# Kernel tuning notes

Measured on AMD Instinct MI355X. Metric: run time of the kernel, lower is better.

The kernel has to match this reference:

```python
import jax, jax.numpy as jnp
import numpy as np
import math

B, T, S = 8, 8, 64
L = T * S            # 512 tokens per modality
D = 1024             # bi_hidden_size
H = 16               # bi_num_attention_heads
DH = D // H          # 64 head size (queries)
DKV = D // 2         # 512 kv projection size
SCALE = 1.0 / math.sqrt(DH)


def setup_inputs() -> dict:
    key = jax.random.key(0)
    ks = jax.random.split(key, 24)
    inp = {
        "input_tensor1": jax.random.normal(ks[0], (B, T, S, D), jnp.float32),
        "attention_mask1": jnp.zeros((B, 1, 1, L), jnp.float32),
        "input_tensor2": jax.random.normal(ks[1], (B, T, S, D), jnp.float32),
        "attention_mask2": jnp.zeros((B, 1, 1, L), jnp.float32),
        "input_tensor3": jax.random.normal(ks[2], (B, T, S, D), jnp.float32),
        "attention_mask3": jnp.zeros((B, 1, 1, L), jnp.float32),
    }
    # Linear params, stored as [in, out]; y = x @ W + b
    kidx = 3
    for i in (1, 2, 3):
        inp[f"w_q{i}"] = jax.random.normal(ks[kidx], (D, D), jnp.float32) * 0.02; kidx += 1
        inp[f"b_q{i}"] = jnp.zeros((D,), jnp.float32)
        inp[f"w_k{i}"] = jax.random.normal(ks[kidx], (D, DKV), jnp.float32) * 0.02; kidx += 1
        inp[f"b_k{i}"] = jnp.zeros((DKV,), jnp.float32)
        inp[f"w_v{i}"] = jax.random.normal(ks[kidx], (D, DKV), jnp.float32) * 0.02; kidx += 1
        inp[f"b_v{i}"] = jnp.zeros((DKV,), jnp.float32)
    return inp


def _heads(x):
    # [B, L, H*dh] -> [B, H, L, dh]
    b, l, d = x.shape
    return x.reshape(b, l, H, d // H).transpose(0, 2, 1, 3)


def _branch(q, k_a, k_b, v_a, v_b, bias):
    # keys/values concatenated along the per-head feature dim (dim 3)
    k = jnp.concatenate([k_a, k_b], axis=-1)          # [B,H,L,dh]
    v = jnp.concatenate([v_a, v_b], axis=-1)          # [B,H,L,dh]
    scores = jnp.einsum('bhqd,bhkd->bhqk', q, k) * SCALE + bias
    probs = jax.nn.softmax(scores, axis=-1)           # [B,H,L,L]
    ctx = jnp.einsum('bhqk,bhkd->bhqd', probs, v)     # [B,H,L,dh]
    ctx = ctx.transpose(0, 2, 1, 3).reshape(q.shape[0], T, S, D)
    return ctx, probs


def reference(input_tensor1, attention_mask1, input_tensor2, attention_mask2,
              input_tensor3, attention_mask3,
              w_q1, b_q1, w_k1, b_k1, w_v1, b_v1,
              w_q2, b_q2, w_k2, b_k2, w_v2, b_v2,
              w_q3, b_q3, w_k3, b_k3, w_v3, b_v3):
    b = input_tensor1.shape[0]
    x1 = input_tensor1.reshape(b, L, -1)
    x2 = input_tensor2.reshape(b, L, -1)
    x3 = input_tensor3.reshape(b, L, -1)
    m1 = attention_mask1.reshape(b, 1, 1, L)
    m2 = attention_mask2.reshape(b, 1, 1, L)
    m3 = attention_mask3.reshape(b, 1, 1, L)

    q1 = _heads(x1 @ w_q1 + b_q1); k1 = _heads(x1 @ w_k1 + b_k1); v1 = _heads(x1 @ w_v1 + b_v1)
    q2 = _heads(x2 @ w_q2 + b_q2); k2 = _heads(x2 @ w_k2 + b_k2); v2 = _heads(x2 @ w_v2 + b_v2)
    q3 = _heads(x3 @ w_q3 + b_q3); k3 = _heads(x3 @ w_k3 + b_k3); v3 = _heads(x3 @ w_v3 + b_v3)

    # branch 1: Q from modality2, KV from 1+3, mask bias from masks 1&3
    c1, p1 = _branch(q2, k1, k3, v1, v3, m1 + m3)
    # branch 2: Q from modality1, KV from 2+3, no mask bias
    c2, p2 = _branch(q1, k2, k3, v2, v3, jnp.zeros((), jnp.float32))
    # branch 3: Q from modality3, KV from 1+2, mask bias from masks 1&2
    c3, p3 = _branch(q3, k1, k2, v1, v2, m1 + m2)

    return (c2, c1, c3, (p2, p1, p3))
```

## Files before the change

### kernel.cpp

```cpp
#include <hip/hip_runtime.h>
#include <hip/hip_bf16.h>

typedef __bf16 bf16x8 __attribute__((ext_vector_type(8)));
typedef float f32x4 __attribute__((ext_vector_type(4)));

#define ATT_SCALE 0.125f

static __device__ __forceinline__ unsigned short f2bf(float f){
  unsigned u = __float_as_uint(f);
  u += 0x7fffu + ((u >> 16) & 1u);
  return (unsigned short)(u >> 16);
}
static __device__ __forceinline__ bf16x8 ld_bf8(const unsigned short* p){
  uint4 u = *(const uint4*)p;
  return __builtin_bit_cast(bf16x8, u);
}
static __device__ __forceinline__ f32x4 mfma16(bf16x8 a, bf16x8 b, f32x4 c){
  return __builtin_amdgcn_mfma_f32_16x16x32_bf16(a, b, c, 0, 0, 0);
}
static __device__ __forceinline__ void gload16(const unsigned short* g, unsigned short* l){
  __builtin_amdgcn_global_load_lds(
      (const __attribute__((address_space(1))) unsigned*)g,
      (__attribute__((address_space(3))) unsigned*)l, 16, 0, 0);
}

struct CastArgs { const float* src[3]; unsigned short* dst[3]; };
__global__ __launch_bounds__(256) void cast_f32_bf16(CastArgs a){
  const float* in = a.src[blockIdx.y];
  unsigned short* out = a.dst[blockIdx.y];
  int i = blockIdx.x*256 + threadIdx.x;
  float4 f = ((const float4*)in)[i];
  ushort4 o = {f2bf(f.x), f2bf(f.y), f2bf(f.z), f2bf(f.w)};
  ((ushort4*)out)[i] = o;
}

struct WtArgs { const float* src[9]; unsigned short* dst[9]; int N[9]; };
__global__ void wtrans(WtArgs a){
  int z = blockIdx.z;
  int N = a.N[z];
  int n0 = blockIdx.x*32;
  if(n0 >= N) return;
  int k0 = blockIdx.y*32;
  const float* W = a.src[z];
  unsigned short* WT = a.dst[z];
  __shared__ float t[32][33];
  int tx = threadIdx.x, ty = threadIdx.y;
  #pragma unroll
  for(int r=0;r<4;++r){
    int row = ty + r*8;
    t[row][tx] = W[(size_t)(k0+row)*N + n0+tx];
  }
  __syncthreads();
  #pragma unroll
  for(int r=0;r<4;++r){
    int row = ty + r*8;
    WT[(size_t)(n0+row)*1024 + k0+tx] = f2bf(t[tx][row]);
  }
}

struct GemmArgs {
  const unsigned short* X[3]; const unsigned short* WT[3];
  const float* bq[3]; const float* bk[3]; const float* bv[3];
  unsigned short* C[3];
};
__global__ __launch_bounds__(256) void gemm_qkv(GemmArgs g){
  __shared__ unsigned short As[128*32];
  __shared__ unsigned short Bs[128*32];
  int z = blockIdx.z;
  const unsigned short* A  = g.X[z];
  const unsigned short* Bt = g.WT[z];
  unsigned short* C = g.C[z];
  int tid = threadIdx.x;
  int wave = tid>>6, lane = tid&63, l15 = lane&15, l4 = lane>>4;
  int m0 = blockIdx.y*128, n0 = blockIdx.x*128;
  int wr = wave>>1, wc = wave&1;
  f32x4 acc[4][4];
  #pragma unroll
  for(int i=0;i<4;++i)
    #pragma unroll
    for(int j=0;j<4;++j) acc[i][j] = (f32x4){0.f,0.f,0.f,0.f};

  int c0r = tid,      row0 = c0r>>2, col0 = (c0r&3)*8;
  int c1r = tid+256,  row1 = c1r>>2, col1 = (c1r&3)*8;
  const unsigned short* a0p = A  + (size_t)(m0+row0)*1024 + col0;
  const unsigned short* a1p = A  + (size_t)(m0+row1)*1024 + col1;
  const unsigned short* b0p = Bt + (size_t)(n0+row0)*1024 + col0;
  const unsigned short* b1p = Bt + (size_t)(n0+row1)*1024 + col1;

  for(int k0=0; k0<1024; k0+=32){
    gload16(a0p + k0, &As[c0r*8]);
    gload16(a1p + k0, &As[c1r*8]);
    gload16(b0p + k0, &Bs[c0r*8]);
    gload16(b1p + k0, &Bs[c1r*8]);
    __syncthreads();
    bf16x8 af[4], bfr[4];
    #pragma unroll
    for(int t=0;t<4;++t){
      af[t]  = ld_bf8(&As[(wr*64 + t*16 + l15)*32 + 8*l4]);
      bfr[t] = ld_bf8(&Bs[(wc*64 + t*16 + l15)*32 + 8*l4]);
    }
    #pragma unroll
    for(int mt=0;mt<4;++mt)
      #pragma unroll
      for(int nt=0;nt<4;++nt)
        acc[mt][nt] = mfma16(af[mt], bfr[nt], acc[mt][nt]);
    __syncthreads();
  }

  #pragma unroll
  for(int mt=0;mt<4;++mt){
    #pragma unroll
    for(int nt=0;nt<4;++nt){
      int col = n0 + wc*64 + nt*16 + l15;
      float bb;
      if(col < 1024)      bb = g.bq[z][col];
      else if(col < 1536) bb = g.bk[z][col-1024];
      else                bb = g.bv[z][col-1536];
      #pragma unroll
      for(int r=0;r<4;++r){
        int row = m0 + wr*64 + mt*16 + l4*4 + r;
        C[(size_t)row*2048 + col] = f2bf(acc[mt][nt][r] + bb);
      }
    }
  }
}

struct VtArgs { const unsigned short* in[3]; unsigned short* out[3]; };
__global__ __launch_bounds__(256) void vtrans(VtArgs a){
  int z = blockIdx.z;
  const unsigned short* in = a.in[z];
  unsigned short* out = a.out[z];
  __shared__ unsigned short T[64][72];
  int r0 = blockIdx.x*64, c0 = blockIdx.y*64;
  int tid = threadIdx.x;
  #pragma unroll
  for(int p=0;p<4;++p){
    int e = p*1024 + tid*4;
    int row = e>>6, col = e&63;
    *(ushort4*)&T[row][col] = *(const ushort4*)&in[(size_t)(r0+row)*2048 + c0+col];
  }
  __syncthreads();
  #pragma unroll
  for(int p=0;p<4;++p){
    int e = p*1024 + tid*4;
    int orow = e>>6, ocol = e&63;
    ushort4 v = {T[ocol][orow], T[ocol+1][orow], T[ocol+2][orow], T[ocol+3][orow]};
    *(ushort4*)&out[(size_t)(c0+orow)*4096 + r0+ocol] = v;
  }
}

struct AttnArgs {
  const unsigned short* Q[3];  const unsigned short* Ka[3]; const unsigned short* Kb[3];
  const unsigned short* VTa[3]; const unsigned short* VTb[3];
  const float* mA[3]; const float* mB[3];
  float* ctx[3]; float* probs[3];
};
__global__ __launch_bounds__(256) void attn(AttnArgs A){
  __shared__ float S[16*512];
  int wg = blockIdx.x;
  int id = (wg & 7)*1536 + (wg >> 3);
  int br = id >> 12;
  int rem = id & 4095;
  int bh = rem >> 5, qt = rem & 31;
  int b = bh >> 4, h = bh & 15;
  const unsigned short* Q   = A.Q[br];
  const unsigned short* Ka  = A.Ka[br];
  const unsigned short* Kb  = A.Kb[br];
  const unsigned short* VTa = A.VTa[br];
  const unsigned short* VTb = A.VTb[br];
  const float* mA = A.mA[br];
  const float* mB = A.mB[br];
  float* ctx   = A.ctx[br];
  float* probs = A.probs[br];

  int tid = threadIdx.x, wave = tid>>6, lane = tid&63, l15 = lane&15, l4 = lane>>4;
  int q0 = qt*16;

  f32x4 msk4[2] = {{0.f,0.f,0.f,0.f},{0.f,0.f,0.f,0.f}};
  #pragma unroll
  for(int it=0; it<2; ++it){
    int c = it*256 + lane*4;
    if(mA) msk4[it] += *(const f32x4*)&mA[b*512 + c];
    if(mB) msk4[it] += *(const f32x4*)&mB[b*512 + c];
  }

  const unsigned short* qp = Q + (size_t)(b*512 + q0 + l15)*2048 + h*64 + 8*l4;
  bf16x8 a0 = ld_bf8(qp);
  bf16x8 a1 = ld_bf8(qp + 32);
  int ct0 = wave*8;
  const unsigned short* kap = Ka + (size_t)(b*512 + ct0*16 + l15)*2048 + h*32 + 8*l4;
  const unsigned short* kbp = Kb + (size_t)(b*512 + ct0*16 + l15)*2048 + h*32 + 8*l4;
  bf16x8 ka[8], kb[8];
  #pragma unroll
  for(int t=0;t<8;++t){
    ka[t] = ld_bf8(kap + (size_t)t*16*2048);
    kb[t] = ld_bf8(kbp + (size_t)t*16*2048);
  }

  int d0 = wave*16 + l15;
  const unsigned short* vb0 = (d0<32 ? VTa + (size_t)(h*32+d0)*4096 : VTb + (size_t)(h*32+d0-32)*4096) + b*512;
  bf16x8 vpre[8];
  #pragma unroll
  for(int kc=0;kc<8;++kc) vpre[kc] = ld_bf8(vb0 + kc*32 + 8*l4);

  #pragma unroll
  for(int t=0;t<8;++t){
    int ct = ct0 + t;
    f32x4 acc = (f32x4){0.f,0.f,0.f,0.f};
    acc = mfma16(a0, ka[t], acc);
    acc = mfma16(a1, kb[t], acc);
    #pragma unroll
    for(int r=0;r<4;++r){
      int row = l4*4 + r;
      int col = ct*16 + l15;
      S[row*512 + ((((col>>2) ^ (row&7)) << 2) | (col&3))] = acc[r];
    }
  }
  __syncthreads();

  for(int rr=0; rr<4; ++rr){
    int r = wave*4 + rr;
    float* rowp = &S[r*512];
    int x = r & 7;
    f32x4 v[2];
    float m = -1e30f;
    #pragma unroll
    for(int it=0; it<2; ++it){
      int c4 = it*64 + lane;
      v[it] = *(const f32x4*)&rowp[(c4 ^ x) << 2];
      v[it] = v[it]*ATT_SCALE + msk4[it];
      m = fmaxf(m, fmaxf(fmaxf(v[it][0], v[it][1]), fmaxf(v[it][2], v[it][3])));
    }
    #pragma unroll
    for(int o=32;o;o>>=1) m = fmaxf(m, __shfl_xor(m, o));
    float sum = 0.f;
    #pragma unroll
    for(int it=0; it<2; ++it){
      #pragma unroll
      for(int j=0;j<4;++j){
        v[it][j] = __expf(v[it][j]-m);
        sum += v[it][j];
      }
    }
    #pragma unroll
    for(int o=32;o;o>>=1) sum += __shfl_xor(sum, o);
    float inv = 1.0f/sum;
    float* po = probs + ((size_t)bh*512 + (q0+r))*512;
    #pragma unroll
    for(int it=0; it<2; ++it){
      int c4 = it*64 + lane;
      f32x4 p = v[it]*inv;
      *(f32x4*)&rowp[(c4 ^ x) << 2] = p;
      *(f32x4*)&po[it*256 + lane*4] = p;
    }
  }
  __syncthreads();

  int px = l15 & 7;
  const float* prowp = &S[l15*512];
  f32x4 accE = (f32x4){0.f,0.f,0.f,0.f}, accO = (f32x4){0.f,0.f,0.f,0.f};
  #pragma unroll
  for(int kc=0;kc<16;++kc){
    int c4a = kc*8 + 2*l4;
    float4 v0 = *(const float4*)&prowp[(c4a ^ px) << 2];
    float4 v1 = *(const float4*)&prowp[((c4a+1) ^ px) << 2];
    bf16x8 a = { (__bf16)v0.x,(__bf16)v0.y,(__bf16)v0.z,(__bf16)v0.w,
                 (__bf16)v1.x,(__bf16)v1.y,(__bf16)v1.z,(__bf16)v1.w };
    bf16x8 bb = (kc < 8) ? vpre[kc] : ld_bf8(vb0 + kc*32 + 8*l4);
    if(kc & 1) accO = mfma16(a, bb, accO);
    else       accE = mfma16(a, bb, accE);
  }
  f32x4 acc = accE + accO;
  #pragma unroll
  for(int r=0;r<4;++r){
    int row = q0 + l4*4 + r;
    ctx[((size_t)(b*512+row))*1024 + h*64 + d0] = acc[r];
  }
}

extern "C" void kernel_launch(void* const* d_in, const int* in_sizes, int n_in,
                              void* d_out, int out_size, void* d_ws, size_t ws_size,
                              hipStream_t stream){
  const float* x[3]    = {(const float*)d_in[0], (const float*)d_in[2], (const float*)d_in[4]};
  const float* mask[3] = {(const float*)d_in[1], (const float*)d_in[3], (const float*)d_in[5]};
  const float *wq[3], *bq[3], *wk[3], *bk[3], *wv[3], *bv[3];
  for(int i=0;i<3;++i){
    wq[i]=(const float*)d_in[6+6*i];  bq[i]=(const float*)d_in[7+6*i];
    wk[i]=(const float*)d_in[8+6*i];  bk[i]=(const float*)d_in[9+6*i];
    wv[i]=(const float*)d_in[10+6*i]; bv[i]=(const float*)d_in[11+6*i];
  }

  unsigned short* ws = (unsigned short*)d_ws;
  unsigned short *Xb[3], *WT[3], *QKV[3], *VT[3];
  for(int i=0;i<3;++i){
    Xb[i]  = ws + (size_t)i*4194304;
    VT[i]  = Xb[i];
    WT[i]  = ws + 12582912 + (size_t)i*2097152;
    QKV[i] = ws + 18874368 + (size_t)i*8388608;
  }

  CastArgs ca;
  for(int i=0;i<3;++i){ ca.src[i]=x[i]; ca.dst[i]=Xb[i]; }
  cast_f32_bf16<<<dim3(4096,3), 256, 0, stream>>>(ca);

  WtArgs wa;
  for(int i=0;i<3;++i){
    wa.src[3*i+0]=wq[i]; wa.dst[3*i+0]=WT[i];           wa.N[3*i+0]=1024;
    wa.src[3*i+1]=wk[i]; wa.dst[3*i+1]=WT[i]+1048576;   wa.N[3*i+1]=512;
    wa.src[3*i+2]=wv[i]; wa.dst[3*i+2]=WT[i]+1572864;   wa.N[3*i+2]=512;
  }
  wtrans<<<dim3(32,32,9), dim3(32,8), 0, stream>>>(wa);

  GemmArgs ga;
  for(int i=0;i<3;++i){
    ga.X[i]=Xb[i]; ga.WT[i]=WT[i]; ga.bq[i]=bq[i]; ga.bk[i]=bk[i]; ga.bv[i]=bv[i]; ga.C[i]=QKV[i];
  }
  gemm_qkv<<<dim3(16,32,3), 256, 0, stream>>>(ga);

  VtArgs va;
  for(int i=0;i<3;++i){ va.in[i]=QKV[i]+1536; va.out[i]=VT[i]; }
  vtrans<<<dim3(64,8,3), 256, 0, stream>>>(va);

  float* out = (float*)d_out;
  float* ctx2 = out;
  float* ctx1 = out + 4194304;
  float* ctx3 = out + 8388608;
  float* p2   = out + 12582912;
  float* p1   = out + 46137344;
  float* p3   = out + 79691776;

  AttnArgs aa;
  aa.Q[0]=QKV[0]; aa.Ka[0]=QKV[1]+1024; aa.Kb[0]=QKV[2]+1024; aa.VTa[0]=VT[1]; aa.VTb[0]=VT[2];
  aa.mA[0]=nullptr; aa.mB[0]=nullptr; aa.ctx[0]=ctx2; aa.probs[0]=p2;
  aa.Q[1]=QKV[1]; aa.Ka[1]=QKV[0]+1024; aa.Kb[1]=QKV[2]+1024; aa.VTa[1]=VT[0]; aa.VTb[1]=VT[2];
  aa.mA[1]=mask[0]; aa.mB[1]=mask[2]; aa.ctx[1]=ctx1; aa.probs[1]=p1;
  aa.Q[2]=QKV[2]; aa.Ka[2]=QKV[0]+1024; aa.Kb[2]=QKV[1]+1024; aa.VTa[2]=VT[0]; aa.VTb[2]=VT[1];
  aa.mA[2]=mask[0]; aa.mB[2]=mask[1]; aa.ctx[2]=ctx3; aa.probs[2]=p3;
  attn<<<12288, 256, 0, stream>>>(aa);
}
```

Before: 332.8 us.

## Double-buffer QKV GEMM LDS tiles and store probs as bf16 in LDS

The QKV projection GEMM now uses two LDS buffers. The next K-tile's global-to-LDS loads are issued before computing on the current tile, and one barrier per iteration is dropped. In the attention kernel, normalized probabilities are packed to bf16 in shared memory with an XOR swizzle, so the PV MFMA loop does one 16-byte LDS load per fragment instead of two float4 loads plus conversions. This adds LDS use in the GEMM, which may affect occupancy. It also relies on an added compiler memory barrier to keep the in-place bf16 writes from overlapping later score-row reads.

Measured after the change: 341.0 us. 2.5% more time.

```diff
diff --git a/kernel.cpp b/kernel.cpp
--- a/kernel.cpp
+++ b/kernel.cpp
@@ -64,8 +64,8 @@
   unsigned short* C[3];
 };
 __global__ __launch_bounds__(256) void gemm_qkv(GemmArgs g){
-  __shared__ unsigned short As[128*32];
-  __shared__ unsigned short Bs[128*32];
+  __shared__ unsigned short As[2][128*32];
+  __shared__ unsigned short Bs[2][128*32];
   int z = blockIdx.z;
   const unsigned short* A  = g.X[z];
   const unsigned short* Bt = g.WT[z];
@@ -87,24 +87,33 @@
   const unsigned short* b0p = Bt + (size_t)(n0+row0)*1024 + col0;
   const unsigned short* b1p = Bt + (size_t)(n0+row1)*1024 + col1;
 
-  for(int k0=0; k0<1024; k0+=32){
-    gload16(a0p + k0, &As[c0r*8]);
-    gload16(a1p + k0, &As[c1r*8]);
-    gload16(b0p + k0, &Bs[c0r*8]);
-    gload16(b1p + k0, &Bs[c1r*8]);
+  gload16(a0p, &As[0][c0r*8]);
+  gload16(a1p, &As[0][c1r*8]);
+  gload16(b0p, &Bs[0][c0r*8]);
+  gload16(b1p, &Bs[0][c1r*8]);
+
+  int cur = 0;
+  for(int t=0; t<32; ++t){
     __syncthreads();
+    if(t+1 < 32){
+      int k0 = (t+1)*32;
+      gload16(a0p + k0, &As[cur^1][c0r*8]);
+      gload16(a1p + k0, &As[cur^1][c1r*8]);
+      gload16(b0p + k0, &Bs[cur^1][c0r*8]);
+      gload16(b1p + k0, &Bs[cur^1][c1r*8]);
+    }
     bf16x8 af[4], bfr[4];
     #pragma unroll
-    for(int t=0;t<4;++t){
-      af[t]  = ld_bf8(&As[(wr*64 + t*16 + l15)*32 + 8*l4]);
-      bfr[t] = ld_bf8(&Bs[(wc*64 + t*16 + l15)*32 + 8*l4]);
+    for(int q=0;q<4;++q){
+      af[q]  = ld_bf8(&As[cur][(wr*64 + q*16 + l15)*32 + 8*l4]);
+      bfr[q] = ld_bf8(&Bs[cur][(wc*64 + q*16 + l15)*32 + 8*l4]);
     }
     #pragma unroll
     for(int mt=0;mt<4;++mt)
       #pragma unroll
       for(int nt=0;nt<4;++nt)
         acc[mt][nt] = mfma16(af[mt], bfr[nt], acc[mt][nt]);
-    __syncthreads();
+    cur ^= 1;
   }
 
   #pragma unroll
@@ -218,6 +227,7 @@
   }
   __syncthreads();
 
+  unsigned short* Pl = (unsigned short*)S;
   for(int rr=0; rr<4; ++rr){
     int r = wave*4 + rr;
     float* rowp = &S[r*512];
@@ -231,6 +241,7 @@
       v[it] = v[it]*ATT_SCALE + msk4[it];
       m = fmaxf(m, fmaxf(fmaxf(v[it][0], v[it][1]), fmaxf(v[it][2], v[it][3])));
     }
+    asm volatile("" ::: "memory");
     #pragma unroll
     for(int o=32;o;o>>=1) m = fmaxf(m, __shfl_xor(m, o));
     float sum = 0.f;
@@ -250,22 +261,21 @@
     for(int it=0; it<2; ++it){
       int c4 = it*64 + lane;
       f32x4 p = v[it]*inv;
-      *(f32x4*)&rowp[(c4 ^ x) << 2] = p;
       *(f32x4*)&po[it*256 + lane*4] = p;
+      int u = c4 >> 1, half = c4 & 1;
+      ushort4 pb = {f2bf(p[0]), f2bf(p[1]), f2bf(p[2]), f2bf(p[3])};
+      *(ushort4*)&Pl[r*1024 + ((u ^ x) << 3) + half*4] = pb;
     }
   }
   __syncthreads();
 
-  int px = l15 & 7;
-  const float* prowp = &S[l15*512];
+  int prx = l15 & 7;
+  const unsigned short* prow = Pl + l15*1024;
   f32x4 accE = (f32x4){0.f,0.f,0.f,0.f}, accO = (f32x4){0.f,0.f,0.f,0.f};
   #pragma unroll
   for(int kc=0;kc<16;++kc){
-    int c4a = kc*8 + 2*l4;
-    float4 v0 = *(const float4*)&prowp[(c4a ^ px) << 2];
-    float4 v1 = *(const float4*)&prowp[((c4a+1) ^ px) << 2];
-    bf16x8 a = { (__bf16)v0.x,(__bf16)v0.y,(__bf16)v0.z,(__bf16)v0.w,
-                 (__bf16)v1.x,(__bf16)v1.y,(__bf16)v1.z,(__bf16)v1.w };
+    int u = kc*4 + l4;
+    bf16x8 a = ld_bf8(prow + ((u ^ prx) << 3));
     bf16x8 bb = (kc < 8) ? vpre[kc] : ld_bf8(vb0 + kc*32 + 8*l4);
     if(kc & 1) accO = mfma16(a, bb, accO);
     else       accE = mfma16(a, bb, accE);
```

## Compute softmax in registers with cross-wave max/sum reduction and bf16 LDS probs

Applied to the files above, without the earlier changes.

The attention kernel now computes scores transposed so each lane holds a query row's column slice in registers. Softmax max and sum are reduced across lanes and then across waves through a small shared array, so the fp32 score matrix no longer round-trips through LDS. Probabilities are written to LDS as swizzled bf16 for the PV MFMA, which halves LDS use and allows a higher occupancy hint (launch_bounds 256,4). The fp32 probs output is written straight from registers at the end. The cost is more register pressure and two extra exps per row.

Result: slower. 367.6 us (+10.5%).

```diff
diff --git a/kernel.cpp b/kernel.cpp
--- a/kernel.cpp
+++ b/kernel.cpp
@@ -155,8 +155,9 @@
   const float* mA[3]; const float* mB[3];
   float* ctx[3]; float* probs[3];
 };
-__global__ __launch_bounds__(256) void attn(AttnArgs A){
-  __shared__ float S[16*512];
+__global__ __launch_bounds__(256,4) void attn(AttnArgs A){
+  __shared__ unsigned short Pl[16*512];
+  __shared__ float2 red[4][16];
   int wg = blockIdx.x;
   int id = (wg & 7)*1536 + (wg >> 3);
   int br = id >> 12;
@@ -175,26 +176,30 @@
 
   int tid = threadIdx.x, wave = tid>>6, lane = tid&63, l15 = lane&15, l4 = lane>>4;
   int q0 = qt*16;
-
-  f32x4 msk4[2] = {{0.f,0.f,0.f,0.f},{0.f,0.f,0.f,0.f}};
-  #pragma unroll
-  for(int it=0; it<2; ++it){
-    int c = it*256 + lane*4;
-    if(mA) msk4[it] += *(const f32x4*)&mA[b*512 + c];
-    if(mB) msk4[it] += *(const f32x4*)&mB[b*512 + c];
-  }
+  int xr = l15 & 7;
 
   const unsigned short* qp = Q + (size_t)(b*512 + q0 + l15)*2048 + h*64 + 8*l4;
   bf16x8 a0 = ld_bf8(qp);
   bf16x8 a1 = ld_bf8(qp + 32);
-  int ct0 = wave*8;
-  const unsigned short* kap = Ka + (size_t)(b*512 + ct0*16 + l15)*2048 + h*32 + 8*l4;
-  const unsigned short* kbp = Kb + (size_t)(b*512 + ct0*16 + l15)*2048 + h*32 + 8*l4;
+
+  int kb0 = wave*128;
+  const unsigned short* kap = Ka + (size_t)(b*512 + kb0 + l15)*2048 + h*32 + 8*l4;
+  const unsigned short* kbp = Kb + (size_t)(b*512 + kb0 + l15)*2048 + h*32 + 8*l4;
   bf16x8 ka[8], kb[8];
   #pragma unroll
   for(int t=0;t<8;++t){
     ka[t] = ld_bf8(kap + (size_t)t*16*2048);
     kb[t] = ld_bf8(kbp + (size_t)t*16*2048);
+  }
+
+  f32x4 msk[8];
+  #pragma unroll
+  for(int t=0;t<8;++t){
+    f32x4 v = (f32x4){0.f,0.f,0.f,0.f};
+    int c = b*512 + kb0 + t*16 + l4*4;
+    if(mA) v += *(const f32x4*)&mA[c];
+    if(mB) v += *(const f32x4*)&mB[c];
+    msk[t] = v;
   }
 
   int d0 = wave*16 + l15;
@@ -203,69 +208,60 @@
   #pragma unroll
   for(int kc=0;kc<8;++kc) vpre[kc] = ld_bf8(vb0 + kc*32 + 8*l4);
 
-  #pragma unroll
-  for(int t=0;t<8;++t){
-    int ct = ct0 + t;
+  f32x4 s[8];
+  #pragma unroll
+  for(int t=0;t<8;++t){
     f32x4 acc = (f32x4){0.f,0.f,0.f,0.f};
-    acc = mfma16(a0, ka[t], acc);
-    acc = mfma16(a1, kb[t], acc);
+    acc = mfma16(ka[t], a0, acc);
+    acc = mfma16(kb[t], a1, acc);
+    s[t] = acc;
+  }
+
+  float m = -1e30f;
+  #pragma unroll
+  for(int t=0;t<8;++t){
+    s[t] = s[t]*ATT_SCALE + msk[t];
+    m = fmaxf(m, fmaxf(fmaxf(s[t][0], s[t][1]), fmaxf(s[t][2], s[t][3])));
+  }
+  m = fmaxf(m, __shfl_xor(m, 16));
+  m = fmaxf(m, __shfl_xor(m, 32));
+  float sum = 0.f;
+  #pragma unroll
+  for(int t=0;t<8;++t){
     #pragma unroll
     for(int r=0;r<4;++r){
-      int row = l4*4 + r;
-      int col = ct*16 + l15;
-      S[row*512 + ((((col>>2) ^ (row&7)) << 2) | (col&3))] = acc[r];
+      s[t][r] = __expf(s[t][r] - m);
+      sum += s[t][r];
     }
   }
+  sum += __shfl_xor(sum, 16);
+  sum += __shfl_xor(sum, 32);
+  if(l4 == 0) red[wave][l15] = make_float2(m, sum);
   __syncthreads();
 
-  for(int rr=0; rr<4; ++rr){
-    int r = wave*4 + rr;
-    float* rowp = &S[r*512];
-    int x = r & 7;
-    f32x4 v[2];
-    float m = -1e30f;
-    #pragma unroll
-    for(int it=0; it<2; ++it){
-      int c4 = it*64 + lane;
-      v[it] = *(const f32x4*)&rowp[(c4 ^ x) << 2];
-      v[it] = v[it]*ATT_SCALE + msk4[it];
-      m = fmaxf(m, fmaxf(fmaxf(v[it][0], v[it][1]), fmaxf(v[it][2], v[it][3])));
-    }
-    #pragma unroll
-    for(int o=32;o;o>>=1) m = fmaxf(m, __shfl_xor(m, o));
-    float sum = 0.f;
-    #pragma unroll
-    for(int it=0; it<2; ++it){
-      #pragma unroll
-      for(int j=0;j<4;++j){
-        v[it][j] = __expf(v[it][j]-m);
-        sum += v[it][j];
-      }
-    }
-    #pragma unroll
-    for(int o=32;o;o>>=1) sum += __shfl_xor(sum, o);
-    float inv = 1.0f/sum;
-    float* po = probs + ((size_t)bh*512 + (q0+r))*512;
-    #pragma unroll
-    for(int it=0; it<2; ++it){
-      int c4 = it*64 + lane;
-      f32x4 p = v[it]*inv;
-      *(f32x4*)&rowp[(c4 ^ x) << 2] = p;
-      *(f32x4*)&po[it*256 + lane*4] = p;
-    }
+  float2 pr0 = red[0][l15], pr1 = red[1][l15], pr2 = red[2][l15], pr3 = red[3][l15];
+  float M = fmaxf(fmaxf(pr0.x, pr1.x), fmaxf(pr2.x, pr3.x));
+  float T = pr0.y*__expf(pr0.x - M) + pr1.y*__expf(pr1.x - M)
+          + pr2.y*__expf(pr2.x - M) + pr3.y*__expf(pr3.x - M);
+  float scale = __expf(m - M) / T;
+
+  #pragma unroll
+  for(int t=0;t<8;++t) s[t] = s[t]*scale;
+
+  #pragma unroll
+  for(int t=0;t<8;++t){
+    int u16 = wave*16 + t*2 + (l4>>1);
+    ushort4 pb = {f2bf(s[t][0]), f2bf(s[t][1]), f2bf(s[t][2]), f2bf(s[t][3])};
+    *(ushort4*)&Pl[l15*512 + ((u16 ^ xr) << 3) + (l4&1)*4] = pb;
   }
   __syncthreads();
 
-  int px = l15 & 7;
-  const float* prowp = &S[l15*512];
+  const unsigned short* prow = Pl + l15*512;
   f32x4 accE = (f32x4){0.f,0.f,0.f,0.f}, accO = (f32x4){0.f,0.f,0.f,0.f};
   #pragma unroll
   for(int kc=0;kc<16;++kc){
-    int c4a = kc*8 + 2*l4;
-    float4 v0 = *(const float4*)&prowp[(c4a ^ px) << 2];
-    float4 v1 = *(const float4*)&prowp[((c4a+1) ^ px) << 2];
-    bf16x8 a = { (__bf16)v0.x,(__bf16)v0.y,(__bf16)v0.z,(__bf16)v0.w,
-                 (__bf16)v1.x,(__bf16)v1.y,(__bf16)v1.z,(__bf16)v1.w };
+    int u = kc*4 + l4;
+    bf16x8 a = ld_bf8(prow + ((u ^ xr) << 3));
     bf16x8 bb = (kc < 8) ? vpre[kc] : ld_bf8(vb0 + kc*32 + 8*l4);
     if(kc & 1) accO = mfma16(a, bb, accO);
     else       accE = mfma16(a, bb, accE);
@@ -276,6 +272,11 @@
     int row = q0 + l4*4 + r;
     ctx[((size_t)(b*512+row))*1024 + h*64 + d0] = acc[r];
   }
+
+  float* po = probs + ((size_t)bh*512 + q0 + l15)*512 + kb0 + l4*4;
+  #pragma unroll
+  for(int t=0;t<8;++t)
+    *(f32x4*)&po[t*16] = s[t];
 }
 
 extern "C" void kernel_launch(void* const* d_in, const int* in_sizes, int n_in,
```

## Fuse fp32-to-bf16 cast into GEMM loads; process two query tiles per attention block

Applied to the files above, without the earlier changes.

Removes the standalone activation cast kernel. The QKV GEMM now loads fp32 activations directly, converts them in registers and writes bf16 to LDS, while the weight tile still uses async global-to-LDS loads. The attention kernel handles two 16-row query tiles per workgroup and reuses the K fragments and preloaded V registers across both, which halves the grid and uses lighter lgkm-only barriers. The trade-offs are synchronous fp32 loads in the GEMM inner loop with more bandwidth per tile, and less parallelism in attention.

Measured after the change: 341.7 us. 2.7% more time.

```diff
diff --git a/kernel.cpp b/kernel.cpp
--- a/kernel.cpp
+++ b/kernel.cpp
@@ -23,15 +23,10 @@
       (const __attribute__((address_space(1))) unsigned*)g,
       (__attribute__((address_space(3))) unsigned*)l, 16, 0, 0);
 }
-
-struct CastArgs { const float* src[3]; unsigned short* dst[3]; };
-__global__ __launch_bounds__(256) void cast_f32_bf16(CastArgs a){
-  const float* in = a.src[blockIdx.y];
-  unsigned short* out = a.dst[blockIdx.y];
-  int i = blockIdx.x*256 + threadIdx.x;
-  float4 f = ((const float4*)in)[i];
-  ushort4 o = {f2bf(f.x), f2bf(f.y), f2bf(f.z), f2bf(f.w)};
-  ((ushort4*)out)[i] = o;
+static __device__ __forceinline__ void lgkm_bar(){
+  asm volatile("s_waitcnt lgkmcnt(0)" ::: "memory");
+  __builtin_amdgcn_s_barrier();
+  __builtin_amdgcn_sched_barrier(0);
 }
 
 struct WtArgs { const float* src[9]; unsigned short* dst[9]; int N[9]; };
@@ -59,7 +54,7 @@
 }
 
 struct GemmArgs {
-  const unsigned short* X[3]; const unsigned short* WT[3];
+  const float* X[3]; const unsigned short* WT[3];
   const float* bq[3]; const float* bk[3]; const float* bv[3];
   unsigned short* C[3];
 };
@@ -67,7 +62,7 @@
   __shared__ unsigned short As[128*32];
   __shared__ unsigned short Bs[128*32];
   int z = blockIdx.z;
-  const unsigned short* A  = g.X[z];
+  const float* A = g.X[z];
   const unsigned short* Bt = g.WT[z];
   unsigned short* C = g.C[z];
   int tid = threadIdx.x;
@@ -82,16 +77,26 @@
 
   int c0r = tid,      row0 = c0r>>2, col0 = (c0r&3)*8;
   int c1r = tid+256,  row1 = c1r>>2, col1 = (c1r&3)*8;
-  const unsigned short* a0p = A  + (size_t)(m0+row0)*1024 + col0;
-  const unsigned short* a1p = A  + (size_t)(m0+row1)*1024 + col1;
+  const float* a0p = A + (size_t)(m0+row0)*1024 + col0;
+  const float* a1p = A + (size_t)(m0+row1)*1024 + col1;
   const unsigned short* b0p = Bt + (size_t)(n0+row0)*1024 + col0;
   const unsigned short* b1p = Bt + (size_t)(n0+row1)*1024 + col1;
 
   for(int k0=0; k0<1024; k0+=32){
-    gload16(a0p + k0, &As[c0r*8]);
-    gload16(a1p + k0, &As[c1r*8]);
     gload16(b0p + k0, &Bs[c0r*8]);
     gload16(b1p + k0, &Bs[c1r*8]);
+    float4 fa0 = *(const float4*)(a0p + k0);
+    float4 fa1 = *(const float4*)(a0p + k0 + 4);
+    float4 fb0 = *(const float4*)(a1p + k0);
+    float4 fb1 = *(const float4*)(a1p + k0 + 4);
+    ushort4 u0 = {f2bf(fa0.x), f2bf(fa0.y), f2bf(fa0.z), f2bf(fa0.w)};
+    ushort4 u1 = {f2bf(fa1.x), f2bf(fa1.y), f2bf(fa1.z), f2bf(fa1.w)};
+    ushort4 u2 = {f2bf(fb0.x), f2bf(fb0.y), f2bf(fb0.z), f2bf(fb0.w)};
+    ushort4 u3 = {f2bf(fb1.x), f2bf(fb1.y), f2bf(fb1.z), f2bf(fb1.w)};
+    *(ushort4*)&As[c0r*8]     = u0;
+    *(ushort4*)&As[c0r*8 + 4] = u1;
+    *(ushort4*)&As[c1r*8]     = u2;
+    *(ushort4*)&As[c1r*8 + 4] = u3;
     __syncthreads();
     bf16x8 af[4], bfr[4];
     #pragma unroll
@@ -158,10 +163,10 @@
 __global__ __launch_bounds__(256) void attn(AttnArgs A){
   __shared__ float S[16*512];
   int wg = blockIdx.x;
-  int id = (wg & 7)*1536 + (wg >> 3);
-  int br = id >> 12;
-  int rem = id & 4095;
-  int bh = rem >> 5, qt = rem & 31;
+  int id = (wg & 7)*768 + (wg >> 3);
+  int br = id >> 11;
+  int rem = id & 2047;
+  int bh = rem >> 4, pr = rem & 15;
   int b = bh >> 4, h = bh & 15;
   const unsigned short* Q   = A.Q[br];
   const unsigned short* Ka  = A.Ka[br];
@@ -174,7 +179,7 @@
   float* probs = A.probs[br];
 
   int tid = threadIdx.x, wave = tid>>6, lane = tid&63, l15 = lane&15, l4 = lane>>4;
-  int q0 = qt*16;
+  int q0A = pr*32;
 
   f32x4 msk4[2] = {{0.f,0.f,0.f,0.f},{0.f,0.f,0.f,0.f}};
   #pragma unroll
@@ -184,9 +189,12 @@
     if(mB) msk4[it] += *(const f32x4*)&mB[b*512 + c];
   }
 
-  const unsigned short* qp = Q + (size_t)(b*512 + q0 + l15)*2048 + h*64 + 8*l4;
-  bf16x8 a0 = ld_bf8(qp);
-  bf16x8 a1 = ld_bf8(qp + 32);
+  const unsigned short* qp = Q + (size_t)(b*512 + q0A + l15)*2048 + h*64 + 8*l4;
+  bf16x8 qa0 = ld_bf8(qp);
+  bf16x8 qa1 = ld_bf8(qp + 32);
+  bf16x8 qb0 = ld_bf8(qp + 16*2048);
+  bf16x8 qb1 = ld_bf8(qp + 16*2048 + 32);
+
   int ct0 = wave*8;
   const unsigned short* kap = Ka + (size_t)(b*512 + ct0*16 + l15)*2048 + h*32 + 8*l4;
   const unsigned short* kbp = Kb + (size_t)(b*512 + ct0*16 + l15)*2048 + h*32 + 8*l4;
@@ -204,77 +212,85 @@
   for(int kc=0;kc<8;++kc) vpre[kc] = ld_bf8(vb0 + kc*32 + 8*l4);
 
   #pragma unroll
-  for(int t=0;t<8;++t){
-    int ct = ct0 + t;
-    f32x4 acc = (f32x4){0.f,0.f,0.f,0.f};
-    acc = mfma16(a0, ka[t], acc);
-    acc = mfma16(a1, kb[t], acc);
+  for(int tile=0; tile<2; ++tile){
+    int q0 = q0A + tile*16;
+    bf16x8 a0 = tile ? qb0 : qa0;
+    bf16x8 a1 = tile ? qb1 : qa1;
+    if(tile) lgkm_bar();
+
+    #pragma unroll
+    for(int t=0;t<8;++t){
+      int ct = ct0 + t;
+      f32x4 acc = (f32x4){0.f,0.f,0.f,0.f};
+      acc = mfma16(a0, ka[t], acc);
+      acc = mfma16(a1, kb[t], acc);
+      #pragma unroll
+      for(int r=0;r<4;++r){
+        int row = l4*4 + r;
+        int col = ct*16 + l15;
+        S[row*512 + ((((col>>2) ^ (row&7)) << 2) | (col&3))] = acc[r];
+      }
+    }
+    lgkm_bar();
+
+    for(int rr=0; rr<4; ++rr){
+      int r = wave*4 + rr;
+      float* rowp = &S[r*512];
+      int x = r & 7;
+      f32x4 v[2];
+      float m = -1e30f;
+      #pragma unroll
+      for(int it=0; it<2; ++it){
+        int c4 = it*64 + lane;
+        v[it] = *(const f32x4*)&rowp[(c4 ^ x) << 2];
+        v[it] = v[it]*ATT_SCALE + msk4[it];
+        m = fmaxf(m, fmaxf(fmaxf(v[it][0], v[it][1]), fmaxf(v[it][2], v[it][3])));
+      }
+      #pragma unroll
+      for(int o=32;o;o>>=1) m = fmaxf(m, __shfl_xor(m, o));
+      float sum = 0.f;
+      #pragma unroll
+      for(int it=0; it<2; ++it){
+        #pragma unroll
+        for(int j=0;j<4;++j){
+          v[it][j] = __expf(v[it][j]-m);
+          sum += v[it][j];
+        }
+      }
+      #pragma unroll
+      for(int o=32;o;o>>=1) sum += __shfl_xor(sum, o);
+      float inv = 1.0f/sum;
+      float* po = probs + ((size_t)bh*512 + (q0+r))*512;
+      #pragma unroll
+      for(int it=0; it<2; ++it){
+        int c4 = it*64 + lane;
+        f32x4 p = v[it]*inv;
+        *(f32x4*)&rowp[(c4 ^ x) << 2] = p;
+        *(f32x4*)&po[it*256 + lane*4] = p;
+      }
+    }
+    lgkm_bar();
+
+    int px = l15 & 7;
+    const float* prowp = &S[l15*512];
+    f32x4 accE = (f32x4){0.f,0.f,0.f,0.f}, accO = (f32x4){0.f,0.f,0.f,0.f};
+    #pragma unroll
+    for(int kc=0;kc<16;++kc){
+      int c4a = kc*8 + 2*l4;
+      float4 v0 = *(const float4*)&prowp[(c4a ^ px) << 2];
+      float4 v1 = *(const float4*)&prowp[((c4a+1) ^ px) << 2];
+      bf16x8 a = { (__bf16)v0.x,(__bf16)v0.y,(__bf16)v0.z,(__bf16)v0.w,
+                   (__bf16)v1.x,(__bf16)v1.y,(__bf16)v1.z,(__bf16)v1.w };
+      bf16x8 bb = (kc < 8) ? vpre[kc] : ld_bf8(vb0 + kc*32 + 8*l4);
+      if(kc & 1) accO = mfma16(a, bb, accO);
+      else       accE = mfma16(a, bb, accE);
+    }
+    f32x4 acc = accE + accO;
     #pragma unroll
     for(int r=0;r<4;++r){
-      int row = l4*4 + r;
-      int col = ct*16 + l15;
-      S[row*512 + ((((col>>2) ^ (row&7)) << 2) | (col&3))] = acc[r];
-    }
-  }
-  __syncthreads();
-
-  for(int rr=0; rr<4; ++rr){
-    int r = wave*4 + rr;
-    float* rowp = &S[r*512];
-    int x = r & 7;
-    f32x4 v[2];
-    float m = -1e30f;
-    #pragma unroll
-    for(int it=0; it<2; ++it){
-      int c4 = it*64 + lane;
-      v[it] = *(const f32x4*)&rowp[(c4 ^ x) << 2];
-      v[it] = v[it]*ATT_SCALE + msk4[it];
-      m = fmaxf(m, fmaxf(fmaxf(v[it][0], v[it][1]), fmaxf(v[it][2], v[it][3])));
-    }
-    #pragma unroll
-    for(int o=32;o;o>>=1) m = fmaxf(m, __shfl_xor(m, o));
-    float sum = 0.f;
-    #pragma unroll
-    for(int it=0; it<2; ++it){
-      #pragma unroll
-      for(int j=0;j<4;++j){
-        v[it][j] = __expf(v[it][j]-m);
-        sum += v[it][j];
-      }
-    }
-    #pragma unroll
-    for(int o=32;o;o>>=1) sum += __shfl_xor(sum, o);
-    float inv = 1.0f/sum;
-    float* po = probs + ((size_t)bh*512 + (q0+r))*512;
-    #pragma unroll
-    for(int it=0; it<2; ++it){
-      int c4 = it*64 + lane;
-      f32x4 p = v[it]*inv;
-      *(f32x4*)&rowp[(c4 ^ x) << 2] = p;
-      *(f32x4*)&po[it*256 + lane*4] = p;
-    }
-  }
-  __syncthreads();
-
-  int px = l15 & 7;
-  const float* prowp = &S[l15*512];
-  f32x4 accE = (f32x4){0.f,0.f,0.f,0.f}, accO = (f32x4){0.f,0.f,0.f,0.f};
-  #pragma unroll
-  for(int kc=0;kc<16;++kc){
-    int c4a = kc*8 + 2*l4;
-    float4 v0 = *(const float4*)&prowp[(c4a ^ px) << 2];
-    float4 v1 = *(const float4*)&prowp[((c4a+1) ^ px) << 2];
-    bf16x8 a = { (__bf16)v0.x,(__bf16)v0.y,(__bf16)v0.z,(__bf16)v0.w,
-                 (__bf16)v1.x,(__bf16)v1.y,(__bf16)v1.z,(__bf16)v1.w };
-    bf16x8 bb = (kc < 8) ? vpre[kc] : ld_bf8(vb0 + kc*32 + 8*l4);
-    if(kc & 1) accO = mfma16(a, bb, accO);
-    else       accE = mfma16(a, bb, accE);
-  }
-  f32x4 acc = accE + accO;
-  #pragma unroll
-  for(int r=0;r<4;++r){
-    int row = q0 + l4*4 + r;
-    ctx[((size_t)(b*512+row))*1024 + h*64 + d0] = acc[r];
+      int row = q0 + l4*4 + r;
+      ctx[((size_t)(b*512+row))*1024 + h*64 + d0] = acc[r];
+    }
   }
 }
 
@@ -291,17 +307,12 @@
   }
 
   unsigned short* ws = (unsigned short*)d_ws;
-  unsigned short *Xb[3], *WT[3], *QKV[3], *VT[3];
+  unsigned short *WT[3], *QKV[3], *VT[3];
   for(int i=0;i<3;++i){
-    Xb[i]  = ws + (size_t)i*4194304;
-    VT[i]  = Xb[i];
+    VT[i]  = ws + (size_t)i*4194304;
     WT[i]  = ws + 12582912 + (size_t)i*2097152;
     QKV[i] = ws + 18874368 + (size_t)i*8388608;
   }
-
-  CastArgs ca;
-  for(int i=0;i<3;++i){ ca.src[i]=x[i]; ca.dst[i]=Xb[i]; }
-  cast_f32_bf16<<<dim3(4096,3), 256, 0, stream>>>(ca);
 
   WtArgs wa;
   for(int i=0;i<3;++i){
@@ -313,7 +324,7 @@
 
   GemmArgs ga;
   for(int i=0;i<3;++i){
-    ga.X[i]=Xb[i]; ga.WT[i]=WT[i]; ga.bq[i]=bq[i]; ga.bk[i]=bk[i]; ga.bv[i]=bv[i]; ga.C[i]=QKV[i];
+    ga.X[i]=x[i]; ga.WT[i]=WT[i]; ga.bq[i]=bq[i]; ga.bk[i]=bk[i]; ga.bv[i]=bv[i]; ga.C[i]=QKV[i];
   }
   gemm_qkv<<<dim3(16,32,3), 256, 0, stream>>>(ga);
 
@@ -336,5 +347,5 @@
   aa.mA[1]=mask[0]; aa.mB[1]=mask[2]; aa.ctx[1]=ctx1; aa.probs[1]=p1;
   aa.Q[2]=QKV[2]; aa.Ka[2]=QKV[0]+1024; aa.Kb[2]=QKV[1]+1024; aa.VTa[2]=VT[0]; aa.VTb[2]=VT[1];
   aa.mA[2]=mask[0]; aa.mB[2]=mask[1]; aa.ctx[2]=ctx3; aa.probs[2]=p3;
-  attn<<<12288, 256, 0, stream>>>(aa);
-}
+  attn<<<6144, 256, 0, stream>>>(aa);
+}
```
